# Performance work log

Measured on AMD Instinct MI355X. Metric: run time of the kernel, lower is better.

## Reference

```python
import jax, jax.numpy as jnp
import numpy as np

B, T, D_MODEL, N_HEADS = 2, 2048, 1024, 16


def setup_inputs() -> dict:
    key = jax.random.key(0)
    ks = jax.random.split(key, 5)
    w_scale = 0.02
    return {
        "x": jax.random.normal(ks[0], (B, T, D_MODEL), jnp.float32),
        "Wq": jax.random.normal(ks[1], (D_MODEL, D_MODEL), jnp.float32) * w_scale,
        "Wk": jax.random.normal(ks[2], (D_MODEL, D_MODEL), jnp.float32) * w_scale,
        "Wv": jax.random.normal(ks[3], (D_MODEL, D_MODEL), jnp.float32) * w_scale,
        "Wo": jax.random.normal(ks[4], (D_MODEL, D_MODEL), jnp.float32) * w_scale,
    }


def reference(x, Wq, Wk, Wv, Wo):
    Bv, Tv, _ = x.shape
    H = N_HEADS
    D = D_MODEL // H
    # Projections (torch nn.Linear: y = x @ W.T), split heads -> (B, H, T, D)
    q = (x @ Wq.T).reshape(Bv, Tv, H, D).transpose(0, 2, 1, 3)
    k = (x @ Wk.T).reshape(Bv, Tv, H, D).transpose(0, 2, 1, 3)
    v = (x @ Wv.T).reshape(Bv, Tv, H, D).transpose(0, 2, 1, 3)

    scale = jnp.sqrt(jnp.asarray(D, jnp.float32))
    scores = jnp.einsum("bhqd,bhkd->bhqk", q, k) / scale  # (B, H, T, T)

    # ALiBi bias: -|i-j| * slope_h, future positions masked to -inf (causal)
    slopes = jnp.asarray(
        [2.0 ** (-8.0 * h / H) for h in range(1, H + 1)], jnp.float32
    )
    pos = jnp.arange(Tv)
    dist = jnp.abs(pos[None, :] - pos[:, None]).astype(jnp.float32)  # (T, T)
    bias = -dist[None, :, :] * slopes[:, None, None]                 # (H, T, T)
    causal_mask = jnp.triu(jnp.ones((Tv, Tv), dtype=bool), 1)
    bias = jnp.where(causal_mask[None, :, :], -jnp.inf, bias)
    scores = scores + bias[None]  # (B, H, T, T)

    attn = jax.nn.softmax(scores, axis=-1)
    out = jnp.einsum("bhqk,bhkd->bhqd", attn, v)
    out = out.transpose(0, 2, 1, 3).reshape(Bv, Tv, D_MODEL)
    return out @ Wo.T
```

## Files before the change

### kernel.cpp

```cpp
#include <hip/hip_runtime.h>


#define DEV __device__ __forceinline__

typedef __attribute__((ext_vector_type(8))) short short8;
typedef __attribute__((ext_vector_type(4))) float f32x4;
typedef __attribute__((ext_vector_type(4))) unsigned short ushort4v;

DEV unsigned short f2bf(float f) {
  unsigned u = __builtin_bit_cast(unsigned, f);
  u += 0x7fffu + ((u >> 16) & 1u);
  return (unsigned short)(u >> 16);
}
DEV float bf2f(unsigned short u) {
  unsigned x = ((unsigned)u) << 16;
  return __builtin_bit_cast(float, x);
}

DEV void gl2lds16(const void* g, void* l) {
  __builtin_amdgcn_global_load_lds(
      (const __attribute__((address_space(1))) void*)g,
      (__attribute__((address_space(3))) void*)l, 16, 0, 0);
}

__global__ __launch_bounds__(256) void cvt_all(
    const float* __restrict__ x, const float* __restrict__ wq,
    const float* __restrict__ wk, const float* __restrict__ wv,
    const float* __restrict__ wo, unsigned short* __restrict__ xb,
    unsigned short* __restrict__ wqb, unsigned short* __restrict__ wkb,
    unsigned short* __restrict__ wvb, unsigned short* __restrict__ wob) {
  int b = blockIdx.x;
  const float* s;
  unsigned short* d;
  int off;
  if (b < 4096)      { s = x;  d = xb;  off = b; }
  else if (b < 5120) { s = wq; d = wqb; off = b - 4096; }
  else if (b < 6144) { s = wk; d = wkb; off = b - 5120; }
  else if (b < 7168) { s = wv; d = wvb; off = b - 6144; }
  else               { s = wo; d = wob; off = b - 7168; }
  int i = (off * 256 + threadIdx.x) * 4;
  float4 v = *(const float4*)(s + i);
  ushort4v o = {f2bf(v.x), f2bf(v.y), f2bf(v.z), f2bf(v.w)};
  *(ushort4v*)(d + i) = o;
}

__global__ __launch_bounds__(512, 2) void gemm_qkv(
    const unsigned short* __restrict__ A, const unsigned short* __restrict__ Wq,
    const unsigned short* __restrict__ Wk, const unsigned short* __restrict__ Wv,
    unsigned short* __restrict__ Qo, unsigned short* __restrict__ Ko,
    unsigned short* __restrict__ Vo) {
  constexpr int K = 1024;
  __shared__ alignas(16) unsigned short Sm[65536];
  const int t = threadIdx.x;
  const int w = t >> 6, l = t & 63, l15 = l & 15, l4 = l >> 4;
  const int wr = w >> 2, wc = w & 3;
  const int wsel = blockIdx.x >> 2;
  const int n0 = (blockIdx.x & 3) * 256;
  const int m0 = blockIdx.y * 256;
  const unsigned short* Bmat = (wsel == 0) ? Wq : ((wsel == 1) ? Wk : Wv);

  const int srow = t >> 3;
  const int sk = ((t & 7) ^ (srow & 7)) * 8;

#define STG_A(T, H)                                                           \
  {                                                                           \
    gl2lds16(A + (m0 + (H)*128 + srow) * K + (T)*64 + sk,                     \
             &Sm[((T)&1) * 16384 + (H)*8192 + t * 8]);                        \
    gl2lds16(A + (m0 + (H)*128 + 64 + srow) * K + (T)*64 + sk,                \
             &Sm[((T)&1) * 16384 + (H)*8192 + 4096 + t * 8]);                 \
  }
#define STG_B(T, H)                                                           \
  {                                                                           \
    gl2lds16(Bmat + (n0 + (H)*128 + srow) * K + (T)*64 + sk,                  \
             &Sm[32768 + ((T)&1) * 16384 + (H)*8192 + t * 8]);                \
    gl2lds16(Bmat + (n0 + (H)*128 + 64 + srow) * K + (T)*64 + sk,             \
             &Sm[32768 + ((T)&1) * 16384 + (H)*8192 + 4096 + t * 8]);         \
  }

  f32x4 acc[8][4];
  {
    f32x4 z4 = {0.f, 0.f, 0.f, 0.f};
#pragma unroll
    for (int i = 0; i < 8; i++)
#pragma unroll
      for (int j = 0; j < 4; j++) acc[i][j] = z4;
  }
  short8 af[4][2], bf[2][2][2];

#define RD_AF(TT, QM)                                                         \
  {                                                                           \
    const unsigned short* Ab_ = &Sm[((TT)&1) * 16384];                        \
    _Pragma("unroll") for (int mi_ = 0; mi_ < 4; mi_++) {                     \
      _Pragma("unroll") for (int kk_ = 0; kk_ < 2; kk_++) {                   \
        af[mi_][kk_] = *(const short8*)&Ab_[                                  \
            (wr * 128 + (QM)*64 + mi_ * 16 + l15) * 64 +                      \
            (((kk_ * 4 + l4) ^ (l15 & 7)) * 8)];                              \
      }                                                                       \
    }                                                                         \
  }
#define RD_BF(TT, QN)                                                         \
  {                                                                           \
    const unsigned short* Bb_ = &Sm[32768 + ((TT)&1) * 16384];                \
    _Pragma("unroll") for (int ni_ = 0; ni_ < 2; ni_++) {                     \
      _Pragma("unroll") for (int kk_ = 0; kk_ < 2; kk_++) {                   \
        bf[(QN)][ni_][kk_] = *(const short8*)&Bb_[                            \
            (wc * 64 + (QN)*32 + ni_ * 16 + l15) * 64 +                       \
            (((kk_ * 4 + l4) ^ (l15 & 7)) * 8)];                              \
      }                                                                       \
    }                                                                         \
  }
#define DO_MFMA(QM, QN)                                                       \
  {                                                                           \
    _Pragma("unroll") for (int mi_ = 0; mi_ < 4; mi_++) {                     \
      _Pragma("unroll") for (int ni_ = 0; ni_ < 2; ni_++) {                   \
        _Pragma("unroll") for (int kk_ = 0; kk_ < 2; kk_++) {                 \
          acc[(QM)*4 + mi_][(QN)*2 + ni_] =                                   \
              __builtin_amdgcn_mfma_f32_16x16x32_bf16(                        \
                  af[mi_][kk_], bf[(QN)][ni_][kk_],                           \
                  acc[(QM)*4 + mi_][(QN)*2 + ni_], 0, 0, 0);                  \
        }                                                                     \
      }                                                                       \
    }                                                                         \
  }

#define VMW4 asm volatile("s_waitcnt vmcnt(4)" ::: "memory")
#define VMW0 asm volatile("s_waitcnt vmcnt(0)" ::: "memory")
#define NOW ((void)0)
#define PHASE(RDS, STG, MFMA_, WAIT)                                          \
  {                                                                           \
    RDS;                                                                      \
    STG;                                                                      \
    __builtin_amdgcn_sched_barrier(0);                                        \
    __builtin_amdgcn_s_barrier();                                             \
    __builtin_amdgcn_s_setprio(1);                                            \
    MFMA_;                                                                    \
    __builtin_amdgcn_s_setprio(0);                                            \
    __builtin_amdgcn_sched_barrier(0);                                        \
    WAIT;                                                                     \
    __builtin_amdgcn_s_barrier();                                             \
  }

  STG_B(0, 0); STG_B(0, 1); STG_A(0, 0); STG_A(0, 1);
  STG_B(1, 0); STG_B(1, 1);
  VMW4;
  __builtin_amdgcn_sched_barrier(0);
  __builtin_amdgcn_s_barrier();

#pragma unroll 1
  for (int i = 0; i < 7; ++i) {
    const int TA = 2 * i, TB = TA + 1;
    PHASE(RD_AF(TA, 0); RD_BF(TA, 0), STG_A(TB, 0),     DO_MFMA(0, 0), NOW);
    PHASE(RD_BF(TA, 1),               STG_A(TB, 1),     DO_MFMA(0, 1), NOW);
    PHASE(RD_AF(TA, 1),               STG_B(TA + 2, 0), DO_MFMA(1, 0), NOW);
    PHASE(NOW,                        STG_B(TA + 2, 1), DO_MFMA(1, 1), VMW4);
    PHASE(RD_AF(TB, 0); RD_BF(TB, 0), STG_A(TA + 2, 0), DO_MFMA(0, 0), NOW);
    PHASE(RD_BF(TB, 1),               STG_A(TA + 2, 1), DO_MFMA(0, 1), NOW);
    PHASE(RD_AF(TB, 1),               STG_B(TB + 2, 0), DO_MFMA(1, 0), NOW);
    PHASE(NOW,                        STG_B(TB + 2, 1), DO_MFMA(1, 1), VMW4);
  }
  PHASE(RD_AF(14, 0); RD_BF(14, 0), STG_A(15, 0), DO_MFMA(0, 0), NOW);
  PHASE(RD_BF(14, 1),               STG_A(15, 1), DO_MFMA(0, 1), NOW);
  PHASE(RD_AF(14, 1),               NOW,          DO_MFMA(1, 0), NOW);
  PHASE(NOW,                        NOW,          DO_MFMA(1, 1), VMW0);
  PHASE(RD_AF(15, 0); RD_BF(15, 0), NOW,          DO_MFMA(0, 0), NOW);
  PHASE(RD_BF(15, 1),               NOW,          DO_MFMA(0, 1), NOW);
  PHASE(RD_AF(15, 1),               NOW,          DO_MFMA(1, 0), NOW);
  PHASE(NOW,                        NOW,          DO_MFMA(1, 1), NOW);

#undef PHASE
#undef NOW
#undef VMW0
#undef VMW4
#undef DO_MFMA
#undef RD_BF
#undef RD_AF
#undef STG_B
#undef STG_A

  if (wsel != 2) {
    unsigned short* D = (wsel == 0) ? Qo : Ko;
    const float scale = (wsel == 0) ? 0.18033688011112042f : 1.0f;
    const int zb = (n0 >> 6) + wc;
#pragma unroll
    for (int mi = 0; mi < 8; mi++)
#pragma unroll
      for (int r = 0; r < 4; r++) {
        int m = m0 + wr * 128 + mi * 16 + l4 * 4 + r;
        int b = m >> 11, tt = m & 2047;
        int z = b * 16 + zb;
#pragma unroll
        for (int ni = 0; ni < 4; ni++)
          D[(z * 2048 + tt) * 64 + ni * 16 + l15] = f2bf(acc[mi][ni][r] * scale);
      }
  } else {
    unsigned short* Tr = Sm + w * 4608;
    const int b = (m0 + wr * 128) >> 11, tbase = (m0 + wr * 128) & 2047;
    const int zg = b * 16 + (n0 >> 6) + wc;
#pragma unroll
    for (int p = 0; p < 2; p++) {
#pragma unroll
      for (int mi = 0; mi < 4; mi++)
#pragma unroll
        for (int ni = 0; ni < 4; ni++) {
          int mg = p * 4 + mi;
          ushort4v pk = {f2bf(acc[mg][ni][0]), f2bf(acc[mg][ni][1]),
                         f2bf(acc[mg][ni][2]), f2bf(acc[mg][ni][3])};
          *(ushort4v*)&Tr[(ni * 16 + l15) * 72 + mi * 16 + l4 * 4] = pk;
        }
      asm volatile("s_waitcnt lgkmcnt(0)" ::: "memory");
      __builtin_amdgcn_sched_barrier(0);
#pragma unroll
      for (int j = 0; j < 8; j++) {
        int idx = j * 64 + l;
        int d = idx >> 3, c = idx & 7;
        short8 v = *(const short8*)&Tr[d * 72 + c * 8];
        *(short8*)&Vo[(zg * 64 + d) * 2048 + tbase + p * 64 + c * 8] = v;
      }
      asm volatile("s_waitcnt lgkmcnt(0)" ::: "memory");
      __builtin_amdgcn_sched_barrier(0);
    }
  }
}

__global__ __launch_bounds__(256, 2) void gemm_o(
    const unsigned short* __restrict__ A, const unsigned short* __restrict__ Bm,
    float* __restrict__ C) {
  constexpr int K = 1024;
  __shared__ alignas(16) unsigned short Al[128 * 32];
  __shared__ alignas(16) unsigned short Bl[64 * 32];
  const int t = threadIdx.x;
  const int l = t & 63, l15 = l & 15, l4 = l >> 4;
  const int wm = ((t >> 6) & 1) * 64, wn = (t >> 7) * 32;
  const int m0 = blockIdx.y * 128, n0 = blockIdx.x * 64;

  f32x4 zero4 = {0.f, 0.f, 0.f, 0.f};
  f32x4 acc[4][2];
#pragma unroll
  for (int i = 0; i < 4; i++)
#pragma unroll
    for (int j = 0; j < 2; j++) acc[i][j] = zero4;

  const int row0 = t >> 2, seg = (t & 3) * 8;
  const unsigned short* Ag0 = A + (m0 + row0) * K + seg;
  const unsigned short* Ag1 = A + (m0 + row0 + 64) * K + seg;
  const unsigned short* Bg0 = Bm + (n0 + row0) * K + seg;

  for (int k0 = 0; k0 < K; k0 += 32) {
    gl2lds16(Ag0 + k0, &Al[t * 8]);
    gl2lds16(Ag1 + k0, &Al[2048 + t * 8]);
    gl2lds16(Bg0 + k0, &Bl[t * 8]);
    __syncthreads();
    short8 af[4], bf2[2];
#pragma unroll
    for (int mi = 0; mi < 4; mi++)
      af[mi] = *(const short8*)&Al[(wm + mi * 16 + l15) * 32 + l4 * 8];
#pragma unroll
    for (int ni = 0; ni < 2; ni++)
      bf2[ni] = *(const short8*)&Bl[(wn + ni * 16 + l15) * 32 + l4 * 8];
#pragma unroll
    for (int mi = 0; mi < 4; mi++)
#pragma unroll
      for (int ni = 0; ni < 2; ni++)
        acc[mi][ni] = __builtin_amdgcn_mfma_f32_16x16x32_bf16(
            af[mi], bf2[ni], acc[mi][ni], 0, 0, 0);
    __syncthreads();
  }
#pragma unroll
  for (int mi = 0; mi < 4; mi++)
#pragma unroll
    for (int r = 0; r < 4; r++) {
      int m = m0 + wm + mi * 16 + l4 * 4 + r;
      float* cp = C + m * 1024 + n0 + wn + l15;
      cp[0] = acc[mi][0][r];
      cp[16] = acc[mi][1][r];
    }
}

__global__ __launch_bounds__(256, 3) void flash_alibi(
    const unsigned short* __restrict__ Q, const unsigned short* __restrict__ Kb,
    const unsigned short* __restrict__ Vt, unsigned short* __restrict__ O0,
    unsigned short* __restrict__ O1, float* __restrict__ L0,
    float* __restrict__ L1) {
  __shared__ alignas(16) unsigned short Kl[2 * 4096];
  __shared__ alignas(16) unsigned short Vl[2 * 4096];
  __shared__ alignas(16) unsigned short Pl[4 * 2304];
  const int t = threadIdx.x, w = t >> 6, l = t & 63, l15 = l & 15, l4 = l >> 4;
  const int g = blockIdx.x;
  const int qt = 15 - (g >> 6);
  const int z = (g & 63) >> 1, s = g & 1;
  const int q0 = qt * 128, h = z & 15;
  const float slope2 = exp2f(-0.5f * (float)(h + 1)) * 1.4426950408889634f;
  const int qrow = q0 + w * 32;

  short8 aq[2][2];
#pragma unroll
  for (int mi = 0; mi < 2; mi++)
#pragma unroll
    for (int ks = 0; ks < 2; ks++)
      aq[mi][ks] = *(const short8*)&Q[(z * 2048 + qrow + mi * 16 + l15) * 64 +
                                      ks * 32 + l4 * 8];

  f32x4 binit[2];
#pragma unroll
  for (int mi = 0; mi < 2; mi++)
#pragma unroll
    for (int r = 0; r < 4; r++)
      binit[mi][r] = -(slope2 * (float)(qrow + mi * 16 + l4 * 4 + r) + 10.0f);

  f32x4 zero4 = {0.f, 0.f, 0.f, 0.f};
  f32x4 o[2][4];
  float lsum[2][4];
#pragma unroll
  for (int mi = 0; mi < 2; mi++)
#pragma unroll
    for (int j = 0; j < 4; j++) {
      o[mi][j] = zero4;
      lsum[mi][j] = 0.f;
    }

  const int row0 = t >> 2, seg8 = (t & 3) * 8;
  const int it0 = s ? (qt + 1) : 0;
  const int nt = qt + 1;

#define ISSUE_LOADS(KV0, BUF)                                                \
  {                                                                          \
    unsigned short* Kd = &Kl[(BUF) * 4096];                                  \
    unsigned short* Vd = &Vl[(BUF) * 4096];                                  \
    gl2lds16(&Kb[(z * 2048 + (KV0) + row0) * 64 + seg8], &Kd[t * 8]);        \
    gl2lds16(&Kb[(z * 2048 + (KV0) + row0) * 64 + 32 + seg8],                \
             &Kd[2048 + t * 8]);                                             \
    gl2lds16(&Vt[(z * 64 + row0) * 2048 + (KV0) + seg8], &Vd[t * 8]);        \
    gl2lds16(&Vt[(z * 64 + row0) * 2048 + (KV0) + 32 + seg8],                \
             &Vd[2048 + t * 8]);                                             \
  }

  ISSUE_LOADS(it0 * 64, 0)

  for (int ii = 0; ii < nt; ++ii) {
    __syncthreads();
    const int kv0 = (it0 + ii) * 64;
    if (ii + 1 < nt) ISSUE_LOADS(kv0 + 64, (ii + 1) & 1)
    if (kv0 > qrow + 31) continue;
    const unsigned short* Kc = &Kl[(ii & 1) * 4096];
    const unsigned short* Vc = &Vl[(ii & 1) * 4096];

    f32x4 sc[2][4];
#pragma unroll
    for (int mi = 0; mi < 2; mi++)
#pragma unroll
      for (int ni = 0; ni < 4; ni++) sc[mi][ni] = binit[mi];
#pragma unroll
    for (int ks = 0; ks < 2; ks++) {
      short8 bk[4];
#pragma unroll
      for (int ni = 0; ni < 4; ni++)
        bk[ni] = *(const short8*)&Kc[(ks * 64 + ni * 16 + l15) * 32 + l4 * 8];
#pragma unroll
      for (int mi = 0; mi < 2; mi++)
#pragma unroll
        for (int ni = 0; ni < 4; ni++)
          sc[mi][ni] = __builtin_amdgcn_mfma_f32_16x16x32_bf16(
              aq[mi][ks], bk[ni], sc[mi][ni], 0, 0, 0);
    }

    const bool needMask = (kv0 + 63 > qrow);
    float jf[4];
#pragma unroll
    for (int ni = 0; ni < 4; ni++) jf[ni] = (float)(kv0 + ni * 16 + l15);

#pragma unroll
    for (int mi = 0; mi < 2; mi++)
#pragma unroll
      for (int r = 0; r < 4; r++) {
        float ps[4];
#pragma unroll
        for (int ni = 0; ni < 4; ni++)
          ps[ni] = __builtin_amdgcn_exp2f(fmaf(slope2, jf[ni], sc[mi][ni][r]));
        if (needMask) {
          int qi = qrow + mi * 16 + l4 * 4 + r;
#pragma unroll
          for (int ni = 0; ni < 4; ni++)
            if (kv0 + ni * 16 + l15 > qi) ps[ni] = 0.f;
        }
        lsum[mi][r] += (ps[0] + ps[1]) + (ps[2] + ps[3]);
        int row = mi * 16 + l4 * 4 + r;
        unsigned short* pp = &Pl[w * 2304 + row * 72 + (l15 & 7)];
#pragma unroll
        for (int ni = 0; ni < 4; ni++)
          pp[((ni * 2 + (l15 >> 3)) ^ l4) * 8] = f2bf(ps[ni]);
      }

    asm volatile("s_waitcnt lgkmcnt(0)" ::: "memory");

    const int rsw = (l15 >> 2) & 3;
#pragma unroll
    for (int ks = 0; ks < 2; ks++) {
      short8 pf[2], vf[4];
#pragma unroll
      for (int mi = 0; mi < 2; mi++)
        pf[mi] = *(const short8*)&Pl[w * 2304 + (mi * 16 + l15) * 72 +
                                     ((ks * 4 + l4) ^ rsw) * 8];
#pragma unroll
      for (int nd = 0; nd < 4; nd++)
        vf[nd] = *(const short8*)&Vc[(ks * 64 + nd * 16 + l15) * 32 + l4 * 8];
#pragma unroll
      for (int mi = 0; mi < 2; mi++)
#pragma unroll
        for (int nd = 0; nd < 4; nd++)
          o[mi][nd] = __builtin_amdgcn_mfma_f32_16x16x32_bf16(
              pf[mi], vf[nd], o[mi][nd], 0, 0, 0);
    }
  }
#undef ISSUE_LOADS

  unsigned short* Op = s ? O1 : O0;
  float* Lp = s ? L1 : L0;
#pragma unroll
  for (int mi = 0; mi < 2; mi++)
#pragma unroll
    for (int r = 0; r < 4; r++) {
      float lv = lsum[mi][r];
#pragma unroll
      for (int off = 1; off < 16; off <<= 1) lv += __shfl_xor(lv, off);
      int tg = qrow + mi * 16 + l4 * 4 + r;
      if (l15 == 0) Lp[z * 2048 + tg] = lv;
      unsigned short* op = &Op[(z * 2048 + tg) * 64 + l15];
#pragma unroll
      for (int nd = 0; nd < 4; nd++) op[nd * 16] = f2bf(o[mi][nd][r]);
    }
}

__global__ __launch_bounds__(256) void combine(
    const unsigned short* __restrict__ O0, const unsigned short* __restrict__ O1,
    const float* __restrict__ L0, const float* __restrict__ L1,
    unsigned short* __restrict__ Ob) {
  int idx = (blockIdx.x * 256 + threadIdx.x) * 8;
  int z = idx >> 17, rem = idx & 131071;
  int tt = rem >> 6, d = rem & 63;
  short8 a = *(const short8*)(O0 + idx);
  short8 b = *(const short8*)(O1 + idx);
  float inv = 1.0f / (L0[z * 2048 + tt] + L1[z * 2048 + tt]);
  short8 o;
#pragma unroll
  for (int j = 0; j < 8; j++) {
    float v = (bf2f((unsigned short)a[j]) + bf2f((unsigned short)b[j])) * inv;
    o[j] = (short)f2bf(v);
  }
  int bq = z >> 4, h = z & 15;
  *(short8*)(Ob + (bq * 2048 + tt) * 1024 + h * 64 + d) = o;
}

extern "C" void kernel_launch(void* const* d_in, const int* in_sizes, int n_in,
                              void* d_out, int out_size, void* d_ws,
                              size_t ws_size, hipStream_t stream) {
  const float* x = (const float*)d_in[0];
  const float* Wq = (const float*)d_in[1];
  const float* Wk = (const float*)d_in[2];
  const float* Wv = (const float*)d_in[3];
  const float* Wo = (const float*)d_in[4];

  char* p = (char*)d_ws;
  unsigned short* xb = (unsigned short*)p;  p += 4096 * 1024 * 2;
  unsigned short* wqb = (unsigned short*)p; p += 1024 * 1024 * 2;
  unsigned short* wkb = (unsigned short*)p; p += 1024 * 1024 * 2;
  unsigned short* wvb = (unsigned short*)p; p += 1024 * 1024 * 2;
  unsigned short* wob = (unsigned short*)p; p += 1024 * 1024 * 2;
  unsigned short* Qb = (unsigned short*)p;  p += 32 * 2048 * 64 * 2;
  unsigned short* Kbf = (unsigned short*)p; p += 32 * 2048 * 64 * 2;
  unsigned short* Vtb = (unsigned short*)p; p += 32 * 2048 * 64 * 2;
  unsigned short* O1 = (unsigned short*)p;  p += 32 * 2048 * 64 * 2;
  float* L0 = (float*)p;                    p += 32 * 2048 * 4;
  float* L1 = (float*)p;                    p += 32 * 2048 * 4;
  unsigned short* O0 = xb;
  unsigned short* Ob = Qb;

  cvt_all<<<8192, 256, 0, stream>>>(x, Wq, Wk, Wv, Wo, xb, wqb, wkb, wvb, wob);
  gemm_qkv<<<dim3(12, 16), 512, 0, stream>>>(xb, wqb, wkb, wvb, Qb, Kbf, Vtb);
  flash_alibi<<<1024, 256, 0, stream>>>(Qb, Kbf, Vtb, O0, O1, L0, L1);
  combine<<<2048, 256, 0, stream>>>(O0, O1, L0, L1, Ob);
  gemm_o<<<dim3(16, 32), 256, 0, stream>>>(Ob, wob, (float*)d_out);
}
```

Measured before the change: 176.3 us.

## Rewrite flash attention with 32x32 MFMA keeping P in registers

```diff
diff --git a/kernel.cpp b/kernel.cpp
--- a/kernel.cpp
+++ b/kernel.cpp
@@ -5,7 +5,9 @@
 
 typedef __attribute__((ext_vector_type(8))) short short8;
 typedef __attribute__((ext_vector_type(4))) float f32x4;
+typedef __attribute__((ext_vector_type(16))) float f32x16;
 typedef __attribute__((ext_vector_type(4))) unsigned short ushort4v;
+typedef __attribute__((ext_vector_type(4))) unsigned uint4v;
 
 DEV unsigned short f2bf(float f) {
   unsigned u = __builtin_bit_cast(unsigned, f);
@@ -15,6 +17,11 @@
 DEV float bf2f(unsigned short u) {
   unsigned x = ((unsigned)u) << 16;
   return __builtin_bit_cast(float, x);
+}
+DEV unsigned cvtpk_bf(float lo, float hi) {
+  unsigned r;
+  asm("v_cvt_pk_bf16_f32 %0, %1, %2" : "=v"(r) : "v"(lo), "v"(hi));
+  return r;
 }
 
 DEV void gl2lds16(const void* g, void* l) {
@@ -213,7 +220,11 @@
       for (int j = 0; j < 8; j++) {
         int idx = j * 64 + l;
         int d = idx >> 3, c = idx & 7;
-        short8 v = *(const short8*)&Tr[d * 72 + c * 8];
+        int t0 = (c >> 1) * 16 + (c & 1) * 4;
+        ushort4v lo4 = *(const ushort4v*)&Tr[d * 72 + t0];
+        ushort4v hi4 = *(const ushort4v*)&Tr[d * 72 + t0 + 8];
+        short8 v = {(short)lo4[0], (short)lo4[1], (short)lo4[2], (short)lo4[3],
+                    (short)hi4[0], (short)hi4[1], (short)hi4[2], (short)hi4[3]};
         *(short8*)&Vo[(zg * 64 + d) * 2048 + tbase + p * 64 + c * 8] = v;
       }
       asm volatile("s_waitcnt lgkmcnt(0)" ::: "memory");
@@ -231,7 +242,8 @@
   const int t = threadIdx.x;
   const int l = t & 63, l15 = l & 15, l4 = l >> 4;
   const int wm = ((t >> 6) & 1) * 64, wn = (t >> 7) * 32;
-  const int m0 = blockIdx.y * 128, n0 = blockIdx.x * 64;
+  const int sblk = (blockIdx.x & 7) * 64 + (blockIdx.x >> 3);
+  const int m0 = (sblk >> 4) * 128, n0 = (sblk & 15) * 64;
 
   f32x4 zero4 = {0.f, 0.f, 0.f, 0.f};
   f32x4 acc[4][2];
@@ -283,55 +295,49 @@
     float* __restrict__ L1) {
   __shared__ alignas(16) unsigned short Kl[2 * 4096];
   __shared__ alignas(16) unsigned short Vl[2 * 4096];
-  __shared__ alignas(16) unsigned short Pl[4 * 2304];
-  const int t = threadIdx.x, w = t >> 6, l = t & 63, l15 = l & 15, l4 = l >> 4;
+  const int t = threadIdx.x, w = t >> 6, l = t & 63;
+  const int l31 = l & 31, h = l >> 5, lsw = l31 & 7;
   const int g = blockIdx.x;
   const int qt = 15 - (g >> 6);
   const int z = (g & 63) >> 1, s = g & 1;
-  const int q0 = qt * 128, h = z & 15;
-  const float slope2 = exp2f(-0.5f * (float)(h + 1)) * 1.4426950408889634f;
+  const int q0 = qt * 128, hd = z & 15;
+  const float slope2 = exp2f(-0.5f * (float)(hd + 1)) * 1.4426950408889634f;
   const int qrow = q0 + w * 32;
-
-  short8 aq[2][2];
-#pragma unroll
-  for (int mi = 0; mi < 2; mi++)
-#pragma unroll
-    for (int ks = 0; ks < 2; ks++)
-      aq[mi][ks] = *(const short8*)&Q[(z * 2048 + qrow + mi * 16 + l15) * 64 +
-                                      ks * 32 + l4 * 8];
-
-  f32x4 binit[2];
-#pragma unroll
-  for (int mi = 0; mi < 2; mi++)
-#pragma unroll
-    for (int r = 0; r < 4; r++)
-      binit[mi][r] = -(slope2 * (float)(qrow + mi * 16 + l4 * 4 + r) + 10.0f);
-
-  f32x4 zero4 = {0.f, 0.f, 0.f, 0.f};
-  f32x4 o[2][4];
-  float lsum[2][4];
-#pragma unroll
-  for (int mi = 0; mi < 2; mi++)
-#pragma unroll
-    for (int j = 0; j < 4; j++) {
-      o[mi][j] = zero4;
-      lsum[mi][j] = 0.f;
-    }
-
-  const int row0 = t >> 2, seg8 = (t & 3) * 8;
+  const int qi = qrow + l31;
+
+  short8 qf[4];
+#pragma unroll
+  for (int ks = 0; ks < 4; ks++)
+    qf[ks] = *(const short8*)&Q[(z * 2048 + qi) * 64 + ks * 16 + h * 8];
+
+  f32x16 binit;
+#pragma unroll
+  for (int r = 0; r < 16; r++)
+    binit[r] =
+        fmaf(slope2, (float)((r & 3) + 8 * (r >> 2) + 4 * h - qi), -10.0f);
+
+  f32x16 accO[2];
+  float lsum = 0.f;
+#pragma unroll
+  for (int nd = 0; nd < 2; nd++)
+#pragma unroll
+    for (int r = 0; r < 16; r++) accO[nd][r] = 0.f;
+
+  const int sr = t >> 3, sgr = t & 7;
   const int it0 = s ? (qt + 1) : 0;
   const int nt = qt + 1;
 
-#define ISSUE_LOADS(KV0, BUF)                                                \
-  {                                                                          \
-    unsigned short* Kd = &Kl[(BUF) * 4096];                                  \
-    unsigned short* Vd = &Vl[(BUF) * 4096];                                  \
-    gl2lds16(&Kb[(z * 2048 + (KV0) + row0) * 64 + seg8], &Kd[t * 8]);        \
-    gl2lds16(&Kb[(z * 2048 + (KV0) + row0) * 64 + 32 + seg8],                \
-             &Kd[2048 + t * 8]);                                             \
-    gl2lds16(&Vt[(z * 64 + row0) * 2048 + (KV0) + seg8], &Vd[t * 8]);        \
-    gl2lds16(&Vt[(z * 64 + row0) * 2048 + (KV0) + 32 + seg8],                \
-             &Vd[2048 + t * 8]);                                             \
+#define ISSUE_LOADS(KV0, BUF)                                                 \
+  {                                                                           \
+    unsigned short* Kd = &Kl[(BUF) * 4096];                                   \
+    unsigned short* Vd = &Vl[(BUF) * 4096];                                   \
+    const int sx = (sgr ^ (sr & 7)) * 8;                                      \
+    gl2lds16(&Kb[(z * 2048 + (KV0) + sr) * 64 + sx], &Kd[t * 8]);             \
+    gl2lds16(&Kb[(z * 2048 + (KV0) + 32 + sr) * 64 + sx],                     \
+             &Kd[2048 + t * 8]);                                              \
+    gl2lds16(&Vt[(z * 64 + sr) * 2048 + (KV0) + sx], &Vd[t * 8]);             \
+    gl2lds16(&Vt[(z * 64 + 32 + sr) * 2048 + (KV0) + sx],                     \
+             &Vd[2048 + t * 8]);                                              \
   }
 
   ISSUE_LOADS(it0 * 64, 0)
@@ -344,89 +350,69 @@
     const unsigned short* Kc = &Kl[(ii & 1) * 4096];
     const unsigned short* Vc = &Vl[(ii & 1) * 4096];
 
-    f32x4 sc[2][4];
-#pragma unroll
-    for (int mi = 0; mi < 2; mi++)
-#pragma unroll
-      for (int ni = 0; ni < 4; ni++) sc[mi][ni] = binit[mi];
-#pragma unroll
-    for (int ks = 0; ks < 2; ks++) {
-      short8 bk[4];
-#pragma unroll
-      for (int ni = 0; ni < 4; ni++)
-        bk[ni] = *(const short8*)&Kc[(ks * 64 + ni * 16 + l15) * 32 + l4 * 8];
-#pragma unroll
-      for (int mi = 0; mi < 2; mi++)
-#pragma unroll
-        for (int ni = 0; ni < 4; ni++)
-          sc[mi][ni] = __builtin_amdgcn_mfma_f32_16x16x32_bf16(
-              aq[mi][ks], bk[ni], sc[mi][ni], 0, 0, 0);
+    f32x16 accS[2];
+    accS[0] = binit;
+    accS[1] = binit;
+#pragma unroll
+    for (int ks = 0; ks < 4; ks++) {
+      short8 kf0 =
+          *(const short8*)&Kc[l31 * 64 + (((ks * 2 + h) ^ lsw) * 8)];
+      short8 kf1 =
+          *(const short8*)&Kc[(32 + l31) * 64 + (((ks * 2 + h) ^ lsw) * 8)];
+      accS[0] = __builtin_amdgcn_mfma_f32_32x32x16_bf16(kf0, qf[ks], accS[0],
+                                                        0, 0, 0);
+      accS[1] = __builtin_amdgcn_mfma_f32_32x32x16_bf16(kf1, qf[ks], accS[1],
+                                                        0, 0, 0);
     }
 
     const bool needMask = (kv0 + 63 > qrow);
-    float jf[4];
-#pragma unroll
-    for (int ni = 0; ni < 4; ni++) jf[ni] = (float)(kv0 + ni * 16 + l15);
-
-#pragma unroll
-    for (int mi = 0; mi < 2; mi++)
-#pragma unroll
-      for (int r = 0; r < 4; r++) {
-        float ps[4];
-#pragma unroll
-        for (int ni = 0; ni < 4; ni++)
-          ps[ni] = __builtin_amdgcn_exp2f(fmaf(slope2, jf[ni], sc[mi][ni][r]));
-        if (needMask) {
-          int qi = qrow + mi * 16 + l4 * 4 + r;
-#pragma unroll
-          for (int ni = 0; ni < 4; ni++)
-            if (kv0 + ni * 16 + l15 > qi) ps[ni] = 0.f;
+#pragma unroll
+    for (int ni = 0; ni < 2; ni++) {
+      const float fkv = (float)(kv0 + 32 * ni);
+      float ps[16];
+#pragma unroll
+      for (int r = 0; r < 16; r++)
+        ps[r] = __builtin_amdgcn_exp2f(fmaf(slope2, fkv, accS[ni][r]));
+      if (needMask) {
+        const int kb = kv0 + 32 * ni + 4 * h;
+#pragma unroll
+        for (int r = 0; r < 16; r++)
+          if (kb + ((r & 3) + 8 * (r >> 2)) > qi) ps[r] = 0.f;
+      }
+      lsum += (((ps[0] + ps[1]) + (ps[2] + ps[3])) +
+               ((ps[4] + ps[5]) + (ps[6] + ps[7]))) +
+              (((ps[8] + ps[9]) + (ps[10] + ps[11])) +
+               ((ps[12] + ps[13]) + (ps[14] + ps[15])));
+      unsigned pk[8];
+#pragma unroll
+      for (int i = 0; i < 8; i++) pk[i] = cvtpk_bf(ps[2 * i], ps[2 * i + 1]);
+#pragma unroll
+      for (int kp = 0; kp < 2; kp++) {
+        uint4v pw = {pk[kp * 4 + 0], pk[kp * 4 + 1], pk[kp * 4 + 2],
+                     pk[kp * 4 + 3]};
+        short8 pa = __builtin_bit_cast(short8, pw);
+#pragma unroll
+        for (int nd = 0; nd < 2; nd++) {
+          short8 vf = *(const short8*)&Vc[(nd * 32 + l31) * 64 +
+                                          ((((ni * 2 + kp) * 2 + h) ^ lsw) * 8)];
+          accO[nd] = __builtin_amdgcn_mfma_f32_32x32x16_bf16(pa, vf, accO[nd],
+                                                             0, 0, 0);
         }
-        lsum[mi][r] += (ps[0] + ps[1]) + (ps[2] + ps[3]);
-        int row = mi * 16 + l4 * 4 + r;
-        unsigned short* pp = &Pl[w * 2304 + row * 72 + (l15 & 7)];
-#pragma unroll
-        for (int ni = 0; ni < 4; ni++)
-          pp[((ni * 2 + (l15 >> 3)) ^ l4) * 8] = f2bf(ps[ni]);
       }
-
-    asm volatile("s_waitcnt lgkmcnt(0)" ::: "memory");
-
-    const int rsw = (l15 >> 2) & 3;
-#pragma unroll
-    for (int ks = 0; ks < 2; ks++) {
-      short8 pf[2], vf[4];
-#pragma unroll
-      for (int mi = 0; mi < 2; mi++)
-        pf[mi] = *(const short8*)&Pl[w * 2304 + (mi * 16 + l15) * 72 +
-                                     ((ks * 4 + l4) ^ rsw) * 8];
-#pragma unroll
-      for (int nd = 0; nd < 4; nd++)
-        vf[nd] = *(const short8*)&Vc[(ks * 64 + nd * 16 + l15) * 32 + l4 * 8];
-#pragma unroll
-      for (int mi = 0; mi < 2; mi++)
-#pragma unroll
-        for (int nd = 0; nd < 4; nd++)
-          o[mi][nd] = __builtin_amdgcn_mfma_f32_16x16x32_bf16(
-              pf[mi], vf[nd], o[mi][nd], 0, 0, 0);
     }
   }
 #undef ISSUE_LOADS
 
   unsigned short* Op = s ? O1 : O0;
   float* Lp = s ? L1 : L0;
-#pragma unroll
-  for (int mi = 0; mi < 2; mi++)
-#pragma unroll
-    for (int r = 0; r < 4; r++) {
-      float lv = lsum[mi][r];
-#pragma unroll
-      for (int off = 1; off < 16; off <<= 1) lv += __shfl_xor(lv, off);
-      int tg = qrow + mi * 16 + l4 * 4 + r;
-      if (l15 == 0) Lp[z * 2048 + tg] = lv;
-      unsigned short* op = &Op[(z * 2048 + tg) * 64 + l15];
-#pragma unroll
-      for (int nd = 0; nd < 4; nd++) op[nd * 16] = f2bf(o[mi][nd][r]);
+  float lv = lsum + __shfl_xor(lsum, 32);
+  if (l < 32) Lp[z * 2048 + qrow + l] = lv;
+#pragma unroll
+  for (int nd = 0; nd < 2; nd++)
+#pragma unroll
+    for (int r = 0; r < 16; r++) {
+      int tg = qrow + (r & 3) + 8 * (r >> 2) + 4 * h;
+      Op[(z * 2048 + tg) * 64 + nd * 32 + l31] = f2bf(accO[nd][r]);
     }
 }
 
@@ -478,5 +464,5 @@
   gemm_qkv<<<dim3(12, 16), 512, 0, stream>>>(xb, wqb, wkb, wvb, Qb, Kbf, Vtb);
   flash_alibi<<<1024, 256, 0, stream>>>(Qb, Kbf, Vtb, O0, O1, L0, L1);
   combine<<<2048, 256, 0, stream>>>(O0, O1, L0, L1, Ob);
-  gemm_o<<<dim3(16, 32), 256, 0, stream>>>(Ob, wob, (float*)d_out);
-}
+  gemm_o<<<512, 256, 0, stream>>>(Ob, wob, (float*)d_out);
+}
```

After: 164.8 us. -6.5%, faster.
